# Kernel optimization log

Measured on AMD Instinct MI355X. Metric: run time of the kernel, lower is better.

## Reference

```python
import jax, jax.numpy as jnp
import numpy as np

B, S, H = 64, 512, 768   # batch, seq_len, biobert-base hidden
E, T = 128, 4            # entities, tokens per entity
NUM_TYPES = 5


def setup_inputs() -> dict:
    key = jax.random.key(0)
    ks = jax.random.split(key, 7)
    return {
        "hidden_states": jax.random.normal(ks[0], (B, S, H), jnp.float32),
        "entity_types": jax.random.randint(ks[1], (B, E), 0, NUM_TYPES, jnp.int32),
        "entity_confidences": jax.random.uniform(ks[2], (B, E), jnp.float32),
        "ent_tokens": jax.random.randint(ks[3], (E, T), 0, S, jnp.int32),
        "type_table": jax.random.normal(ks[4], (NUM_TYPES, H), jnp.float32),
        "conf_w": jax.random.normal(ks[5], (1, H), jnp.float32) * 0.02,
        "conf_b": jax.random.normal(ks[6], (H,), jnp.float32) * 0.02,
    }


def reference(hidden_states, entity_types, entity_confidences, ent_tokens,
              type_table, conf_w, conf_b):
    # entity embedding = type embedding + confidence projection (dropout = eval identity)
    type_emb = type_table[entity_types]                                  # [B,E,H]
    conf_emb = entity_confidences[..., None] * conf_w[0] + conf_b        # [B,E,H]
    entity_emb = type_emb + conf_emb                                     # [B,E,H]

    # scatter-add entity embedding into every token position of that entity
    e, t = ent_tokens.shape
    flat_idx = ent_tokens.reshape(-1)                                    # [E*T]
    add = jnp.repeat(entity_emb, t, axis=1)                              # [B,E*T,H]
    enhanced = hidden_states.at[:, flat_idx].add(add)                    # [B,S,H]

    # per-entity mean pooling over the entity's (enhanced) token embeddings
    gathered = enhanced[:, ent_tokens]                                   # [B,E,T,H]
    entity_embeddings = gathered.mean(axis=2)                            # [B,E,H]
    return enhanced, entity_embeddings
```

## Files before the change

kernel.cpp:

```cpp
#include <hip/hip_runtime.h>

#define BB 64
#define SS 512
#define HH 768
#define EE 128
#define TT 4

__global__ __launch_bounds__(SS) void build_index_kernel(
    const int* __restrict__ ent_tokens,
    int* __restrict__ offsets,
    int* __restrict__ entries) {
    __shared__ int cnt[SS];
    __shared__ int scan[SS];
    __shared__ int pos[SS];
    const int tid = threadIdx.x;

    cnt[tid] = 0;
    __syncthreads();

    const int s = ent_tokens[tid];
    atomicAdd(&cnt[s], 1);
    __syncthreads();

    scan[tid] = cnt[tid];
    __syncthreads();
    for (int off = 1; off < SS; off <<= 1) {
        int add = (tid >= off) ? scan[tid - off] : 0;
        __syncthreads();
        scan[tid] += add;
        __syncthreads();
    }

    const int excl = scan[tid] - cnt[tid];
    offsets[tid] = excl;
    if (tid == 0) offsets[SS] = EE * TT;
    pos[tid] = excl;
    __syncthreads();

    const int p = atomicAdd(&pos[s], 1);
    entries[p] = tid >> 2;
}

__global__ __launch_bounds__(HH / 4) void enhance_kernel(
    const float* __restrict__ hidden,
    const int* __restrict__ entity_types,
    const float* __restrict__ conf,
    const float* __restrict__ type_table,
    const float* __restrict__ conf_w,
    const float* __restrict__ conf_b,
    const int* __restrict__ offsets,
    const int* __restrict__ entries,
    float* __restrict__ enhanced) {
    const int row = blockIdx.x;
    const int b = row >> 9;
    const int s = row & (SS - 1);
    const int h4 = threadIdx.x;

    float4 acc = ((const float4*)(hidden + (size_t)row * HH))[h4];

    const int o0 = offsets[s];
    const int o1 = offsets[s + 1];
    if (o1 > o0) {
        const float4 wv = ((const float4*)conf_w)[h4];
        const float4 bv = ((const float4*)conf_b)[h4];
        for (int j = o0; j < o1; ++j) {
            const int e = entries[j];
            const int ty = entity_types[b * EE + e];
            const float c = conf[b * EE + e];
            const float4 tv = ((const float4*)(type_table + (size_t)ty * HH))[h4];
            acc.x += tv.x + fmaf(c, wv.x, bv.x);
            acc.y += tv.y + fmaf(c, wv.y, bv.y);
            acc.z += tv.z + fmaf(c, wv.z, bv.z);
            acc.w += tv.w + fmaf(c, wv.w, bv.w);
        }
    }

    ((float4*)(enhanced + (size_t)row * HH))[h4] = acc;
}

__global__ __launch_bounds__(HH / 4) void gather_mean_kernel(
    const float* __restrict__ enhanced,
    const int* __restrict__ ent_tokens,
    float* __restrict__ ee) {
    const int be = blockIdx.x;
    const int b = be >> 7;
    const int e = be & (EE - 1);
    const int h4 = threadIdx.x;

    float4 acc = make_float4(0.f, 0.f, 0.f, 0.f);
    for (int t = 0; t < TT; ++t) {
        const int s = ent_tokens[e * TT + t];
        const float4 v =
            ((const float4*)(enhanced + ((size_t)(b * SS + s)) * HH))[h4];
        acc.x += v.x;
        acc.y += v.y;
        acc.z += v.z;
        acc.w += v.w;
    }
    float4 o;
    o.x = acc.x * 0.25f;
    o.y = acc.y * 0.25f;
    o.z = acc.z * 0.25f;
    o.w = acc.w * 0.25f;
    ((float4*)(ee + (size_t)be * HH))[h4] = o;
}

extern "C" void kernel_launch(void* const* d_in, const int* in_sizes, int n_in,
                              void* d_out, int out_size, void* d_ws,
                              size_t ws_size, hipStream_t stream) {
    const float* hidden = (const float*)d_in[0];
    const int* entity_types = (const int*)d_in[1];
    const float* conf = (const float*)d_in[2];
    const int* ent_tokens = (const int*)d_in[3];
    const float* type_table = (const float*)d_in[4];
    const float* conf_w = (const float*)d_in[5];
    const float* conf_b = (const float*)d_in[6];

    float* enhanced = (float*)d_out;
    float* ee = (float*)d_out + (size_t)BB * SS * HH;

    int* offsets = (int*)d_ws;
    int* entries = offsets + (SS + 1);

    build_index_kernel<<<1, SS, 0, stream>>>(ent_tokens, offsets, entries);
    enhance_kernel<<<BB * SS, HH / 4, 0, stream>>>(
        hidden, entity_types, conf, type_table, conf_w, conf_b, offsets,
        entries, enhanced);
    gather_mean_kernel<<<BB * EE, HH / 4, 0, stream>>>(enhanced, ent_tokens, ee);
}
```

Before: 225.8 us.

## Fuse index build, enhance, and gather-mean into a single kernel launch

```diff
diff --git a/kernel.cpp b/kernel.cpp
--- a/kernel.cpp
+++ b/kernel.cpp
@@ -5,126 +5,130 @@
 #define HH 768
 #define EE 128
 #define TT 4
+#define NP (EE * TT)
+#define H4 (HH / 4)
+#define NPAIRBLK (BB * EE)
+#define NROWBLK (BB * SS)
 
-__global__ __launch_bounds__(SS) void build_index_kernel(
-    const int* __restrict__ ent_tokens,
-    int* __restrict__ offsets,
-    int* __restrict__ entries) {
-    __shared__ int cnt[SS];
-    __shared__ int scan[SS];
-    __shared__ int pos[SS];
-    const int tid = threadIdx.x;
+typedef float vf4 __attribute__((ext_vector_type(4)));
 
-    cnt[tid] = 0;
-    __syncthreads();
-
-    const int s = ent_tokens[tid];
-    atomicAdd(&cnt[s], 1);
-    __syncthreads();
-
-    scan[tid] = cnt[tid];
-    __syncthreads();
-    for (int off = 1; off < SS; off <<= 1) {
-        int add = (tid >= off) ? scan[tid - off] : 0;
-        __syncthreads();
-        scan[tid] += add;
-        __syncthreads();
-    }
-
-    const int excl = scan[tid] - cnt[tid];
-    offsets[tid] = excl;
-    if (tid == 0) offsets[SS] = EE * TT;
-    pos[tid] = excl;
-    __syncthreads();
-
-    const int p = atomicAdd(&pos[s], 1);
-    entries[p] = tid >> 2;
-}
-
-__global__ __launch_bounds__(HH / 4) void enhance_kernel(
+__global__ __launch_bounds__(H4) void mega_kernel(
     const float* __restrict__ hidden,
     const int* __restrict__ entity_types,
     const float* __restrict__ conf,
+    const int* __restrict__ ent_tokens,
     const float* __restrict__ type_table,
     const float* __restrict__ conf_w,
     const float* __restrict__ conf_b,
-    const int* __restrict__ offsets,
-    const int* __restrict__ entries,
-    float* __restrict__ enhanced) {
-    const int row = blockIdx.x;
-    const int b = row >> 9;
-    const int s = row & (SS - 1);
-    const int h4 = threadIdx.x;
+    float* __restrict__ enhanced,
+    float* __restrict__ ee) {
+  __shared__ int ltok[NP];
+  __shared__ int ml[NP];
+  __shared__ int nm;
 
-    float4 acc = ((const float4*)(hidden + (size_t)row * HH))[h4];
+  const int tid = threadIdx.x;
 
-    const int o0 = offsets[s];
-    const int o1 = offsets[s + 1];
-    if (o1 > o0) {
-        const float4 wv = ((const float4*)conf_w)[h4];
-        const float4 bv = ((const float4*)conf_b)[h4];
-        for (int j = o0; j < o1; ++j) {
-            const int e = entries[j];
-            const int ty = entity_types[b * EE + e];
-            const float c = conf[b * EE + e];
-            const float4 tv = ((const float4*)(type_table + (size_t)ty * HH))[h4];
-            acc.x += tv.x + fmaf(c, wv.x, bv.x);
-            acc.y += tv.y + fmaf(c, wv.y, bv.y);
-            acc.z += tv.z + fmaf(c, wv.z, bv.z);
-            acc.w += tv.w + fmaf(c, wv.w, bv.w);
-        }
+  ltok[tid] = ent_tokens[tid];
+  ltok[tid + 192] = ent_tokens[tid + 192];
+  if (tid < NP - 384) ltok[tid + 384] = ent_tokens[tid + 384];
+
+  const float4 wv = ((const float4*)conf_w)[tid];
+  const float4 bv = ((const float4*)conf_b)[tid];
+
+  if (blockIdx.x < NPAIRBLK) {
+    const int b = blockIdx.x >> 7;
+    const int e = blockIdx.x & (EE - 1);
+    const int bE = b * EE;
+
+    float4 aee = make_float4(0.f, 0.f, 0.f, 0.f);
+
+    for (int t = 0; t < TT; ++t) {
+      if (tid == 0) nm = 0;
+      __syncthreads();
+
+      const int s = ltok[e * TT + t];
+      if (ltok[tid] == s) ml[atomicAdd(&nm, 1)] = tid;
+      if (ltok[tid + 192] == s) ml[atomicAdd(&nm, 1)] = tid + 192;
+      if (tid < 128 && ltok[tid + 384] == s) ml[atomicAdd(&nm, 1)] = tid + 384;
+      __syncthreads();
+
+      const int cnt = nm;
+      float4 acc = ((const float4*)(hidden + ((size_t)(b * SS + s)) * HH))[tid];
+      for (int m = 0; m < cnt; ++m) {
+        const int p = ml[m];
+        const int ei = p >> 2;
+        const int ty = entity_types[bE + ei];
+        const float c = conf[bE + ei];
+        const float4 tv = ((const float4*)(type_table + (size_t)ty * HH))[tid];
+        acc.x += tv.x + fmaf(c, wv.x, bv.x);
+        acc.y += tv.y + fmaf(c, wv.y, bv.y);
+        acc.z += tv.z + fmaf(c, wv.z, bv.z);
+        acc.w += tv.w + fmaf(c, wv.w, bv.w);
+      }
+      aee.x += acc.x;
+      aee.y += acc.y;
+      aee.z += acc.z;
+      aee.w += acc.w;
+      __syncthreads();
     }
 
-    ((float4*)(enhanced + (size_t)row * HH))[h4] = acc;
-}
+    vf4 o;
+    o.x = aee.x * 0.25f;
+    o.y = aee.y * 0.25f;
+    o.z = aee.z * 0.25f;
+    o.w = aee.w * 0.25f;
+    __builtin_nontemporal_store(o, (vf4*)(ee + (size_t)(bE + e) * HH) + tid);
+  } else {
+    const int r = blockIdx.x - NPAIRBLK;
+    const int b = r >> 9;
+    const int s = r & (SS - 1);
+    const int bE = b * EE;
 
-__global__ __launch_bounds__(HH / 4) void gather_mean_kernel(
-    const float* __restrict__ enhanced,
-    const int* __restrict__ ent_tokens,
-    float* __restrict__ ee) {
-    const int be = blockIdx.x;
-    const int b = be >> 7;
-    const int e = be & (EE - 1);
-    const int h4 = threadIdx.x;
+    if (tid == 0) nm = 0;
+    __syncthreads();
 
-    float4 acc = make_float4(0.f, 0.f, 0.f, 0.f);
-    for (int t = 0; t < TT; ++t) {
-        const int s = ent_tokens[e * TT + t];
-        const float4 v =
-            ((const float4*)(enhanced + ((size_t)(b * SS + s)) * HH))[h4];
-        acc.x += v.x;
-        acc.y += v.y;
-        acc.z += v.z;
-        acc.w += v.w;
+    if (ltok[tid] == s) ml[atomicAdd(&nm, 1)] = tid;
+    if (ltok[tid + 192] == s) ml[atomicAdd(&nm, 1)] = tid + 192;
+    if (tid < 128 && ltok[tid + 384] == s) ml[atomicAdd(&nm, 1)] = tid + 384;
+    __syncthreads();
+
+    const int cnt = nm;
+    float4 acc = ((const float4*)(hidden + (size_t)r * HH))[tid];
+    for (int m = 0; m < cnt; ++m) {
+      const int p = ml[m];
+      const int ei = p >> 2;
+      const int ty = entity_types[bE + ei];
+      const float c = conf[bE + ei];
+      const float4 tv = ((const float4*)(type_table + (size_t)ty * HH))[tid];
+      acc.x += tv.x + fmaf(c, wv.x, bv.x);
+      acc.y += tv.y + fmaf(c, wv.y, bv.y);
+      acc.z += tv.z + fmaf(c, wv.z, bv.z);
+      acc.w += tv.w + fmaf(c, wv.w, bv.w);
     }
-    float4 o;
-    o.x = acc.x * 0.25f;
-    o.y = acc.y * 0.25f;
-    o.z = acc.z * 0.25f;
-    o.w = acc.w * 0.25f;
-    ((float4*)(ee + (size_t)be * HH))[h4] = o;
+    vf4 ov;
+    ov.x = acc.x;
+    ov.y = acc.y;
+    ov.z = acc.z;
+    ov.w = acc.w;
+    __builtin_nontemporal_store(ov, (vf4*)(enhanced + (size_t)r * HH) + tid);
+  }
 }
 
 extern "C" void kernel_launch(void* const* d_in, const int* in_sizes, int n_in,
                               void* d_out, int out_size, void* d_ws,
                               size_t ws_size, hipStream_t stream) {
-    const float* hidden = (const float*)d_in[0];
-    const int* entity_types = (const int*)d_in[1];
-    const float* conf = (const float*)d_in[2];
-    const int* ent_tokens = (const int*)d_in[3];
-    const float* type_table = (const float*)d_in[4];
-    const float* conf_w = (const float*)d_in[5];
-    const float* conf_b = (const float*)d_in[6];
+  const float* hidden = (const float*)d_in[0];
+  const int* entity_types = (const int*)d_in[1];
+  const float* conf = (const float*)d_in[2];
+  const int* ent_tokens = (const int*)d_in[3];
+  const float* type_table = (const float*)d_in[4];
+  const float* conf_w = (const float*)d_in[5];
+  const float* conf_b = (const float*)d_in[6];
 
-    float* enhanced = (float*)d_out;
-    float* ee = (float*)d_out + (size_t)BB * SS * HH;
+  float* enhanced = (float*)d_out;
+  float* ee = (float*)d_out + (size_t)BB * SS * HH;
 
-    int* offsets = (int*)d_ws;
-    int* entries = offsets + (SS + 1);
-
-    build_index_kernel<<<1, SS, 0, stream>>>(ent_tokens, offsets, entries);
-    enhance_kernel<<<BB * SS, HH / 4, 0, stream>>>(
-        hidden, entity_types, conf, type_table, conf_w, conf_b, offsets,
-        entries, enhanced);
-    gather_mean_kernel<<<BB * EE, HH / 4, 0, stream>>>(enhanced, ent_tokens, ee);
+  mega_kernel<<<NPAIRBLK + NROWBLK, H4, 0, stream>>>(
+      hidden, entity_types, conf, ent_tokens, type_table, conf_w, conf_b,
+      enhanced, ee);
 }
```

Result: slower. 232.2 us (+2.8%).

## Fuse enhance and gather-mean into one kernel recomputing pooled means from hidden

Applied to the files above, without the earlier changes.

```diff
diff --git a/kernel.cpp b/kernel.cpp
--- a/kernel.cpp
+++ b/kernel.cpp
@@ -5,126 +5,177 @@
 #define HH 768
 #define EE 128
 #define TT 4
+#define NP (EE * TT)
+#define H4 (HH / 4)
+#define NF4_ROWS (BB * SS * H4)
+#define NF4_EE (BB * EE * H4)
+#define TPB 256
+#define PART2_BLKS (NF4_EE / TPB)
+#define PART1_BLKS (NF4_ROWS / (TPB * 4))
+
+typedef float vf4 __attribute__((ext_vector_type(4)));
 
 __global__ __launch_bounds__(SS) void build_index_kernel(
-    const int* __restrict__ ent_tokens,
-    int* __restrict__ offsets,
+    const int* __restrict__ ent_tokens, int* __restrict__ offsets,
     int* __restrict__ entries) {
-    __shared__ int cnt[SS];
-    __shared__ int scan[SS];
-    __shared__ int pos[SS];
-    const int tid = threadIdx.x;
+  __shared__ int cnt[SS];
+  __shared__ int scan[SS];
+  __shared__ int pos[SS];
+  const int tid = threadIdx.x;
 
-    cnt[tid] = 0;
+  cnt[tid] = 0;
+  __syncthreads();
+  const int s = ent_tokens[tid];
+  atomicAdd(&cnt[s], 1);
+  __syncthreads();
+
+  scan[tid] = cnt[tid];
+  __syncthreads();
+  for (int off = 1; off < SS; off <<= 1) {
+    int add = (tid >= off) ? scan[tid - off] : 0;
     __syncthreads();
+    scan[tid] += add;
+    __syncthreads();
+  }
 
-    const int s = ent_tokens[tid];
-    atomicAdd(&cnt[s], 1);
-    __syncthreads();
+  const int excl = scan[tid] - cnt[tid];
+  offsets[tid] = excl;
+  if (tid == 0) offsets[SS] = NP;
+  pos[tid] = excl;
+  __syncthreads();
 
-    scan[tid] = cnt[tid];
-    __syncthreads();
-    for (int off = 1; off < SS; off <<= 1) {
-        int add = (tid >= off) ? scan[tid - off] : 0;
-        __syncthreads();
-        scan[tid] += add;
-        __syncthreads();
-    }
-
-    const int excl = scan[tid] - cnt[tid];
-    offsets[tid] = excl;
-    if (tid == 0) offsets[SS] = EE * TT;
-    pos[tid] = excl;
-    __syncthreads();
-
-    const int p = atomicAdd(&pos[s], 1);
-    entries[p] = tid >> 2;
+  const int p = atomicAdd(&pos[s], 1);
+  entries[p] = tid >> 2;
 }
 
-__global__ __launch_bounds__(HH / 4) void enhance_kernel(
+__global__ __launch_bounds__(TPB) void fused_kernel(
     const float* __restrict__ hidden,
     const int* __restrict__ entity_types,
     const float* __restrict__ conf,
+    const int* __restrict__ ent_tokens,
     const float* __restrict__ type_table,
     const float* __restrict__ conf_w,
     const float* __restrict__ conf_b,
     const int* __restrict__ offsets,
     const int* __restrict__ entries,
-    float* __restrict__ enhanced) {
-    const int row = blockIdx.x;
-    const int b = row >> 9;
-    const int s = row & (SS - 1);
-    const int h4 = threadIdx.x;
+    float* __restrict__ enhanced,
+    float* __restrict__ ee) {
+  const int tid = threadIdx.x;
 
-    float4 acc = ((const float4*)(hidden + (size_t)row * HH))[h4];
+  if (blockIdx.x < PART2_BLKS) {
+    const int idx = blockIdx.x * TPB + tid;
+    const int be = idx / H4;
+    const int col = idx - be * H4;
+    const int b = be >> 7;
+    const int e = be & (EE - 1);
+    const int bE = b * EE;
 
-    const int o0 = offsets[s];
-    const int o1 = offsets[s + 1];
-    if (o1 > o0) {
-        const float4 wv = ((const float4*)conf_w)[h4];
-        const float4 bv = ((const float4*)conf_b)[h4];
-        for (int j = o0; j < o1; ++j) {
-            const int e = entries[j];
-            const int ty = entity_types[b * EE + e];
-            const float c = conf[b * EE + e];
-            const float4 tv = ((const float4*)(type_table + (size_t)ty * HH))[h4];
-            acc.x += tv.x + fmaf(c, wv.x, bv.x);
-            acc.y += tv.y + fmaf(c, wv.y, bv.y);
-            acc.z += tv.z + fmaf(c, wv.z, bv.z);
-            acc.w += tv.w + fmaf(c, wv.w, bv.w);
-        }
+    const int4 tok = ((const int4*)ent_tokens)[e];
+    const float* hb = hidden + (size_t)b * SS * HH;
+    const float4 h0 = ((const float4*)(hb + (size_t)tok.x * HH))[col];
+    const float4 h1 = ((const float4*)(hb + (size_t)tok.y * HH))[col];
+    const float4 h2 = ((const float4*)(hb + (size_t)tok.z * HH))[col];
+    const float4 h3 = ((const float4*)(hb + (size_t)tok.w * HH))[col];
+    const float4 wv = ((const float4*)conf_w)[col];
+    const float4 bv = ((const float4*)conf_b)[col];
+
+    float4 acc;
+    acc.x = (h0.x + h1.x) + (h2.x + h3.x);
+    acc.y = (h0.y + h1.y) + (h2.y + h3.y);
+    acc.z = (h0.z + h1.z) + (h2.z + h3.z);
+    acc.w = (h0.w + h1.w) + (h2.w + h3.w);
+
+    const int toks[TT] = {tok.x, tok.y, tok.z, tok.w};
+#pragma unroll
+    for (int t = 0; t < TT; ++t) {
+      const int s = toks[t];
+      const int o0 = offsets[s];
+      const int o1 = offsets[s + 1];
+      for (int j = o0; j < o1; ++j) {
+        const int ei = entries[j];
+        const int ty = entity_types[bE + ei];
+        const float c = conf[bE + ei];
+        const float4 tv = ((const float4*)(type_table + (size_t)ty * HH))[col];
+        acc.x += tv.x + fmaf(c, wv.x, bv.x);
+        acc.y += tv.y + fmaf(c, wv.y, bv.y);
+        acc.z += tv.z + fmaf(c, wv.z, bv.z);
+        acc.w += tv.w + fmaf(c, wv.w, bv.w);
+      }
     }
 
-    ((float4*)(enhanced + (size_t)row * HH))[h4] = acc;
-}
-
-__global__ __launch_bounds__(HH / 4) void gather_mean_kernel(
-    const float* __restrict__ enhanced,
-    const int* __restrict__ ent_tokens,
-    float* __restrict__ ee) {
-    const int be = blockIdx.x;
-    const int b = be >> 7;
-    const int e = be & (EE - 1);
-    const int h4 = threadIdx.x;
-
-    float4 acc = make_float4(0.f, 0.f, 0.f, 0.f);
-    for (int t = 0; t < TT; ++t) {
-        const int s = ent_tokens[e * TT + t];
-        const float4 v =
-            ((const float4*)(enhanced + ((size_t)(b * SS + s)) * HH))[h4];
-        acc.x += v.x;
-        acc.y += v.y;
-        acc.z += v.z;
-        acc.w += v.w;
-    }
-    float4 o;
+    vf4 o;
     o.x = acc.x * 0.25f;
     o.y = acc.y * 0.25f;
     o.z = acc.z * 0.25f;
     o.w = acc.w * 0.25f;
-    ((float4*)(ee + (size_t)be * HH))[h4] = o;
+    __builtin_nontemporal_store(o, (vf4*)ee + idx);
+  } else {
+    const int base = (blockIdx.x - PART2_BLKS) * (TPB * 4) + tid;
+    float4 hv[4];
+    int rows[4], cols[4];
+#pragma unroll
+    for (int j = 0; j < 4; ++j) {
+      const int idx = base + TPB * j;
+      rows[j] = idx / H4;
+      cols[j] = idx - rows[j] * H4;
+      hv[j] = ((const float4*)hidden)[idx];
+    }
+#pragma unroll
+    for (int j = 0; j < 4; ++j) {
+      const int idx = base + TPB * j;
+      const int r = rows[j];
+      const int col = cols[j];
+      const int b = r >> 9;
+      const int s = r & (SS - 1);
+      const int bE = b * EE;
+
+      float4 acc = hv[j];
+      const int o0 = offsets[s];
+      const int o1 = offsets[s + 1];
+      if (o1 > o0) {
+        const float4 wv = ((const float4*)conf_w)[col];
+        const float4 bv = ((const float4*)conf_b)[col];
+        for (int m = o0; m < o1; ++m) {
+          const int ei = entries[m];
+          const int ty = entity_types[bE + ei];
+          const float c = conf[bE + ei];
+          const float4 tv =
+              ((const float4*)(type_table + (size_t)ty * HH))[col];
+          acc.x += tv.x + fmaf(c, wv.x, bv.x);
+          acc.y += tv.y + fmaf(c, wv.y, bv.y);
+          acc.z += tv.z + fmaf(c, wv.z, bv.z);
+          acc.w += tv.w + fmaf(c, wv.w, bv.w);
+        }
+      }
+      vf4 ov;
+      ov.x = acc.x;
+      ov.y = acc.y;
+      ov.z = acc.z;
+      ov.w = acc.w;
+      __builtin_nontemporal_store(ov, (vf4*)enhanced + idx);
+    }
+  }
 }
 
 extern "C" void kernel_launch(void* const* d_in, const int* in_sizes, int n_in,
                               void* d_out, int out_size, void* d_ws,
                               size_t ws_size, hipStream_t stream) {
-    const float* hidden = (const float*)d_in[0];
-    const int* entity_types = (const int*)d_in[1];
-    const float* conf = (const float*)d_in[2];
-    const int* ent_tokens = (const int*)d_in[3];
-    const float* type_table = (const float*)d_in[4];
-    const float* conf_w = (const float*)d_in[5];
-    const float* conf_b = (const float*)d_in[6];
+  const float* hidden = (const float*)d_in[0];
+  const int* entity_types = (const int*)d_in[1];
+  const float* conf = (const float*)d_in[2];
+  const int* ent_tokens = (const int*)d_in[3];
+  const float* type_table = (const float*)d_in[4];
+  const float* conf_w = (const float*)d_in[5];
+  const float* conf_b = (const float*)d_in[6];
 
-    float* enhanced = (float*)d_out;
-    float* ee = (float*)d_out + (size_t)BB * SS * HH;
+  float* enhanced = (float*)d_out;
+  float* ee = (float*)d_out + (size_t)BB * SS * HH;
 
-    int* offsets = (int*)d_ws;
-    int* entries = offsets + (SS + 1);
+  int* offsets = (int*)d_ws;
+  int* entries = offsets + (SS + 1);
 
-    build_index_kernel<<<1, SS, 0, stream>>>(ent_tokens, offsets, entries);
-    enhance_kernel<<<BB * SS, HH / 4, 0, stream>>>(
-        hidden, entity_types, conf, type_table, conf_w, conf_b, offsets,
-        entries, enhanced);
-    gather_mean_kernel<<<BB * EE, HH / 4, 0, stream>>>(enhanced, ent_tokens, ee);
+  build_index_kernel<<<1, SS, 0, stream>>>(ent_tokens, offsets, entries);
+  fused_kernel<<<PART2_BLKS + PART1_BLKS, TPB, 0, stream>>>(
+      hidden, entity_types, conf, ent_tokens, type_table, conf_w, conf_b,
+      offsets, entries, enhanced, ee);
 }
```

Result: slower. 234.2 us (+3.7%).
